# Kernel optimization log

Measured on AMD Instinct MI355X. Metric: run time of the kernel, lower is better.

Reference implementation:

```python
import jax, jax.numpy as jnp
import numpy as np

EPS = 1e-5


def _conv(x, w, padding, groups=1):
    return jax.lax.conv_general_dilated(
        x, w, window_strides=(1, 1),
        padding=[(padding, padding), (padding, padding)],
        dimension_numbers=("NCHW", "OIHW", "NCHW"),
        feature_group_count=groups)


def _bn(x, gamma, beta, mean, var):
    # inference-mode BatchNorm2d, params shape [C]
    inv = gamma * jax.lax.rsqrt(var + EPS)
    return x * inv[None, :, None, None] + (beta - mean * inv)[None, :, None, None]


def _adder_dw(x, w):
    # depthwise AdderNet 'conv': out[b, c*R+r, h, w] = -sum_{kh,kw} |x[b,c,h+kh-p,w+kw-p] - w[c,r,kh,kw]|
    # x: [B,C,H,W], w: [C,R,K,K] (groups=C, R outputs per group)
    B, C, H, W = x.shape
    R, K = w.shape[1], w.shape[-1]
    p = K // 2
    xp = jnp.pad(x, ((0, 0), (0, 0), (p, p), (p, p)))
    acc = jnp.zeros((B, C, R, H, W), x.dtype)
    for kh in range(K):          # fixed small 3x3 tap loop
        for kw in range(K):
            shift = xp[:, :, kh:kh + H, kw:kw + W]          # [B,C,H,W]
            tap = w[:, :, kh, kw]                           # [C,R]
            acc = acc + jnp.abs(shift[:, :, None] - tap[None, :, :, None, None])
    return -acc.reshape(B, C * R, H, W)


def setup_inputs() -> dict:
    key = jax.random.key(0)
    ks = jax.random.split(key, 12)
    B, Cin, H, W = 32, 240, 56, 56
    init_c, ratio = 24, 10
    r1 = ratio - 1            # 9 ghost channels per primary channel
    new_c = init_c * r1       # 216
    f32 = jnp.float32
    x = jax.random.normal(ks[0], (B, Cin, H, W), f32)
    w_primary = jax.random.normal(ks[1], (init_c, Cin, 1, 1), f32) * 0.05
    w_dw = jax.random.normal(ks[2], (init_c, 1, 3, 3), f32) * 0.1
    w_add = jax.random.normal(ks[3], (init_c, r1, 3, 3), f32) * 0.1
    def bn(kk, c):
        k1, k2 = jax.random.split(kk)
        return (jnp.ones((c,), f32), jnp.zeros((c,), f32),
                jax.random.normal(k1, (c,), f32) * 0.1,
                jax.random.uniform(k2, (c,), f32, 0.5, 1.5))
    g1, b1, m1, v1 = bn(ks[4], init_c)
    g2, b2, m2, v2 = bn(ks[5], init_c)
    g3, b3, m3, v3 = bn(ks[6], new_c)
    return dict(x=x, w_primary=w_primary, g1=g1, b1=b1, m1=m1, v1=v1,
                w_dw=w_dw, g2=g2, b2=b2, m2=m2, v2=v2,
                w_add=w_add, g3=g3, b3=b3, m3=m3, v3=v3)


def reference(x, w_primary, g1, b1, m1, v1, w_dw, g2, b2, m2, v2,
              w_add, g3, b3, m3, v3):
    oup = 240
    init_c = w_primary.shape[0]
    # primary_conv: 1x1 conv -> BN -> depthwise 3x3 conv -> BN -> Identity (relu slot is Identity)
    x1 = _conv(x, w_primary, padding=0)
    x1 = _bn(x1, g1, b1, m1, v1)
    x1 = _conv(x1, w_dw, padding=1, groups=init_c)
    x1 = _bn(x1, g2, b2, m2, v2)
    # cheap_operation: depthwise Adder2D -> BN -> ReLU
    x2 = _adder_dw(x1, w_add)
    x2 = jax.nn.relu(_bn(x2, g3, b3, m3, v3))
    out = jnp.concatenate([x1, x2], axis=1)
    return out[:, :oup]
```

## Files before the change

### kernel.cpp

```cpp
#include <hip/hip_runtime.h>

#define EPS_ 1e-5f
#define BATCH 32
#define CIN 240
#define H_ 56
#define W_ 56
#define HW 3136
#define C1 24
#define R_ 9
#define C2 216
#define COUT 240

#define WS_WT   0
#define WS_B1   5760
#define WS_WDW  5784
#define WS_B2   6000
#define WS_INV3 6024
#define WS_T3   6240

__global__ __launch_bounds__(256) void prep_kernel(
    const float* __restrict__ wp,
    const float* __restrict__ g1, const float* __restrict__ b1,
    const float* __restrict__ m1, const float* __restrict__ v1,
    const float* __restrict__ wdw,
    const float* __restrict__ g2, const float* __restrict__ b2,
    const float* __restrict__ m2, const float* __restrict__ v2,
    const float* __restrict__ g3, const float* __restrict__ b3,
    const float* __restrict__ m3, const float* __restrict__ v3,
    float* __restrict__ ws) {
  int i = blockIdx.x * 256 + threadIdx.x;
  if (i < 5760) {
    int ci = i / C1, co = i % C1;
    float s = g1[co] / sqrtf(v1[co] + EPS_);
    ws[WS_WT + ci * C1 + co] = wp[co * CIN + ci] * s;
    if (ci == 0) ws[WS_B1 + co] = b1[co] - m1[co] * s;
  } else if (i < 5760 + C2) {
    int j = i - 5760;
    int c = j / 9;
    float s = g2[c] / sqrtf(v2[c] + EPS_);
    ws[WS_WDW + j] = wdw[j] * s;
    if (j % 9 == 0) ws[WS_B2 + c] = b2[c] - m2[c] * s;
  } else if (i < 5976 + C2) {
    int j = i - 5976;
    float s = g3[j] / sqrtf(v3[j] + EPS_);
    ws[WS_INV3 + j] = s;
    ws[WS_T3 + j] = b3[j] - m3[j] * s;
  }
}

__global__ __launch_bounds__(256, 2) void conv1x1_kernel(
    const float* __restrict__ x, const float* __restrict__ wt,
    const float* __restrict__ bias1, float* __restrict__ out) {
  __shared__ float smem[12288];
  const int tid  = threadIdx.x;
  const int lane = tid & 63;
  const int wv   = tid >> 6;

  for (int i = tid; i < 5760; i += 256) smem[i] = wt[i];
  __syncthreads();

  const int P  = blockIdx.x * 256 + lane * 4;
  const int b  = P / HW;
  const int hw = P - b * HW;
  const int ci0 = wv * 60;
  const float* xp = x + ((size_t)b * CIN + ci0) * HW + hw;

  float acc[96];
#pragma unroll
  for (int i = 0; i < 96; ++i) acc[i] = 0.f;

  float4 A[6], B[6];
#pragma unroll
  for (int j = 0; j < 6; ++j) A[j] = *(const float4*)(xp + (size_t)j * HW);
#pragma unroll
  for (int j = 0; j < 6; ++j) B[j] = *(const float4*)(xp + (size_t)(6 + j) * HW);

  auto fmachunk = [&](const float4* buf, int cbase) {
#pragma unroll
    for (int j = 0; j < 6; ++j) {
      const float4 xv = buf[j];
      const float* wr = &smem[(ci0 + cbase + j) * C1];
#pragma unroll
      for (int k = 0; k < 6; ++k) {
        const float4 wq = *(const float4*)(wr + 4 * k);
        const int o = 16 * k;
        acc[o+ 0] = fmaf(wq.x, xv.x, acc[o+ 0]);
        acc[o+ 1] = fmaf(wq.x, xv.y, acc[o+ 1]);
        acc[o+ 2] = fmaf(wq.x, xv.z, acc[o+ 2]);
        acc[o+ 3] = fmaf(wq.x, xv.w, acc[o+ 3]);
        acc[o+ 4] = fmaf(wq.y, xv.x, acc[o+ 4]);
        acc[o+ 5] = fmaf(wq.y, xv.y, acc[o+ 5]);
        acc[o+ 6] = fmaf(wq.y, xv.z, acc[o+ 6]);
        acc[o+ 7] = fmaf(wq.y, xv.w, acc[o+ 7]);
        acc[o+ 8] = fmaf(wq.z, xv.x, acc[o+ 8]);
        acc[o+ 9] = fmaf(wq.z, xv.y, acc[o+ 9]);
        acc[o+10] = fmaf(wq.z, xv.z, acc[o+10]);
        acc[o+11] = fmaf(wq.z, xv.w, acc[o+11]);
        acc[o+12] = fmaf(wq.w, xv.x, acc[o+12]);
        acc[o+13] = fmaf(wq.w, xv.y, acc[o+13]);
        acc[o+14] = fmaf(wq.w, xv.z, acc[o+14]);
        acc[o+15] = fmaf(wq.w, xv.w, acc[o+15]);
      }
    }
  };

#pragma unroll 1
  for (int g = 0; g < 4; ++g) {
    const int c = 12 * g;
    fmachunk(A, c);
#pragma unroll
    for (int j = 0; j < 6; ++j)
      A[j] = *(const float4*)(xp + (size_t)(c + 12 + j) * HW);
    fmachunk(B, c + 6);
#pragma unroll
    for (int j = 0; j < 6; ++j)
      B[j] = *(const float4*)(xp + (size_t)(c + 18 + j) * HW);
  }
  fmachunk(A, 48);
  fmachunk(B, 54);
  __syncthreads();

  float* red0 = smem;
  float* red1 = smem + 6144;

  if (wv == 2) {
#pragma unroll
    for (int i = 0; i < 96; ++i) red0[i * 64 + lane] = acc[i];
  } else if (wv == 3) {
#pragma unroll
    for (int i = 0; i < 96; ++i) red1[i * 64 + lane] = acc[i];
  }
  __syncthreads();
  if (wv == 0) {
#pragma unroll
    for (int i = 0; i < 96; ++i) acc[i] += red0[i * 64 + lane];
  } else if (wv == 1) {
#pragma unroll
    for (int i = 0; i < 96; ++i) acc[i] += red1[i * 64 + lane];
  }
  __syncthreads();
  if (wv == 1) {
#pragma unroll
    for (int i = 0; i < 96; ++i) red0[i * 64 + lane] = acc[i];
  }
  __syncthreads();
  if (wv == 0) {
    float* o = out + ((size_t)b * COUT + C1) * HW + hw;
#pragma unroll
    for (int co = 0; co < C1; ++co) {
      const float bb = bias1[co];
      float4 v;
      v.x = acc[co*4+0] + red0[(co*4+0)*64 + lane] + bb;
      v.y = acc[co*4+1] + red0[(co*4+1)*64 + lane] + bb;
      v.z = acc[co*4+2] + red0[(co*4+2)*64 + lane] + bb;
      v.w = acc[co*4+3] + red0[(co*4+3)*64 + lane] + bb;
      *(float4*)(o + (size_t)co * HW) = v;
    }
  }
}

__global__ __launch_bounds__(256) void dw_kernel(
    const float* __restrict__ outr, const float* __restrict__ wdwf,
    const float* __restrict__ bias2, float* __restrict__ out) {
  const int c = blockIdx.y, b = blockIdx.z;
  const int q = blockIdx.x * 256 + threadIdx.x;
  if (q >= 784) return;
  const int h  = q / 14;
  const int w0 = (q - h * 14) * 4;
  const float* in = outr + ((size_t)b * COUT + C1 + c) * HW;

  float wk[9];
#pragma unroll
  for (int k = 0; k < 9; ++k) wk[k] = wdwf[c * 9 + k];
  const float bb = bias2[c];

  float xr[3][6];
#pragma unroll
  for (int kh = 0; kh < 3; ++kh) {
    const int hh = h + kh - 1;
    const bool rok = (hh >= 0) & (hh < H_);
    const float* rp = in + hh * W_;
    xr[kh][0] = (rok && w0 > 0) ? rp[w0 - 1] : 0.f;
    if (rok) {
      const float4 m = *(const float4*)(rp + w0);
      xr[kh][1] = m.x; xr[kh][2] = m.y; xr[kh][3] = m.z; xr[kh][4] = m.w;
    } else {
      xr[kh][1] = 0.f; xr[kh][2] = 0.f; xr[kh][3] = 0.f; xr[kh][4] = 0.f;
    }
    xr[kh][5] = (rok && w0 < W_ - 4) ? rp[w0 + 4] : 0.f;
  }

  float4 v = {bb, bb, bb, bb};
#pragma unroll
  for (int kh = 0; kh < 3; ++kh) {
#pragma unroll
    for (int kw = 0; kw < 3; ++kw) {
      const float t = wk[kh * 3 + kw];
      v.x = fmaf(xr[kh][kw + 0], t, v.x);
      v.y = fmaf(xr[kh][kw + 1], t, v.y);
      v.z = fmaf(xr[kh][kw + 2], t, v.z);
      v.w = fmaf(xr[kh][kw + 3], t, v.w);
    }
  }
  *(float4*)(out + ((size_t)b * COUT + c) * HW + h * W_ + w0) = v;
}

__global__ __launch_bounds__(256) void adder_kernel(
    const float* __restrict__ outr, const float* __restrict__ wadd,
    const float* __restrict__ inv3, const float* __restrict__ t3,
    float* __restrict__ out) {
  const int c = blockIdx.y, b = blockIdx.z;
  __shared__ float taps[R_][3][4];
  __shared__ float s3[R_], t3s[R_];
  const int tid = threadIdx.x;
  if (tid < 108) {
    int r = tid / 12, kh = (tid / 4) % 3, kw = tid & 3;
    taps[r][kh][kw] = (kw < 3) ? wadd[((c * R_ + r) * 3 + kh) * 3 + kw] : 0.f;
  } else if (tid >= 128 && tid < 128 + R_) {
    int r = tid - 128;
    s3[r]  = inv3[c * R_ + r];
    t3s[r] = t3[c * R_ + r];
  }
  __syncthreads();

  const int q = blockIdx.x * 256 + tid;
  if (q >= 784) return;
  const int h  = q / 14;
  const int w0 = (q - h * 14) * 4;
  const float* in = outr + ((size_t)b * COUT + c) * HW;

  float xr[3][6];
#pragma unroll
  for (int kh = 0; kh < 3; ++kh) {
    const int hh = h + kh - 1;
    const bool rok = (hh >= 0) & (hh < H_);
    const float* rp = in + hh * W_;
    xr[kh][0] = (rok && w0 > 0) ? rp[w0 - 1] : 0.f;
    if (rok) {
      const float4 m = *(const float4*)(rp + w0);
      xr[kh][1] = m.x; xr[kh][2] = m.y; xr[kh][3] = m.z; xr[kh][4] = m.w;
    } else {
      xr[kh][1] = 0.f; xr[kh][2] = 0.f; xr[kh][3] = 0.f; xr[kh][4] = 0.f;
    }
    xr[kh][5] = (rok && w0 < W_ - 4) ? rp[w0 + 4] : 0.f;
  }

#pragma unroll
  for (int r = 0; r < R_; ++r) {
    float a0 = 0.f, a1 = 0.f, a2 = 0.f, a3 = 0.f;
#pragma unroll
    for (int kh = 0; kh < 3; ++kh) {
#pragma unroll
      for (int kw = 0; kw < 3; ++kw) {
        const float t = taps[r][kh][kw];
        a0 += fabsf(xr[kh][kw + 0] - t);
        a1 += fabsf(xr[kh][kw + 1] - t);
        a2 += fabsf(xr[kh][kw + 2] - t);
        a3 += fabsf(xr[kh][kw + 3] - t);
      }
    }
    const float s = s3[r], bb = t3s[r];
    float4 v;
    v.x = fmaxf(fmaf(-s, a0, bb), 0.f);
    v.y = fmaxf(fmaf(-s, a1, bb), 0.f);
    v.z = fmaxf(fmaf(-s, a2, bb), 0.f);
    v.w = fmaxf(fmaf(-s, a3, bb), 0.f);
    *(float4*)(out + ((size_t)b * COUT + C1 + c * R_ + r) * HW + h * W_ + w0) = v;
  }
}

extern "C" void kernel_launch(void* const* d_in, const int* in_sizes, int n_in,
                              void* d_out, int out_size, void* d_ws, size_t ws_size,
                              hipStream_t stream) {
  const float* x    = (const float*)d_in[0];
  const float* wp   = (const float*)d_in[1];
  const float* g1   = (const float*)d_in[2];
  const float* b1   = (const float*)d_in[3];
  const float* m1   = (const float*)d_in[4];
  const float* v1   = (const float*)d_in[5];
  const float* wdw  = (const float*)d_in[6];
  const float* g2   = (const float*)d_in[7];
  const float* b2   = (const float*)d_in[8];
  const float* m2   = (const float*)d_in[9];
  const float* v2   = (const float*)d_in[10];
  const float* wadd = (const float*)d_in[11];
  const float* g3   = (const float*)d_in[12];
  const float* b3   = (const float*)d_in[13];
  const float* m3   = (const float*)d_in[14];
  const float* v3   = (const float*)d_in[15];

  float* ws  = (float*)d_ws;
  float* out = (float*)d_out;

  prep_kernel<<<25, 256, 0, stream>>>(wp, g1, b1, m1, v1, wdw, g2, b2, m2, v2,
                                      g3, b3, m3, v3, ws);

  conv1x1_kernel<<<392, 256, 0, stream>>>(x, ws + WS_WT, ws + WS_B1, out);

  dw_kernel<<<dim3(4, C1, BATCH), 256, 0, stream>>>(out, ws + WS_WDW,
                                                    ws + WS_B2, out);

  adder_kernel<<<dim3(4, C1, BATCH), 256, 0, stream>>>(out, wadd, ws + WS_INV3,
                                                       ws + WS_T3, out);
}
```

Measured before the change: 227.7 us.

## Split conv1x1 output channels across wave pairs to halve accumulators per thread

The 1x1 conv block grows from 256 to 512 threads. Each pair of waves shares one 60-channel K slice and splits the 24 output channels into two halves of 12, so each thread holds 48 accumulators instead of 96. Shared memory drops to 6144 floats and the launch bounds rise to (512,4), aiming for more resident waves to hide the global load latency on x. In exchange, every x value is loaded by two waves (doubling global/L2 reads of the input) and the cross-wave reduction takes more sync steps.

```diff
diff --git a/kernel.cpp b/kernel.cpp
--- a/kernel.cpp
+++ b/kernel.cpp
@@ -48,40 +48,43 @@
   }
 }
 
-__global__ __launch_bounds__(256, 2) void conv1x1_kernel(
+__global__ __launch_bounds__(512, 4) void conv1x1_kernel(
     const float* __restrict__ x, const float* __restrict__ wt,
     const float* __restrict__ bias1, float* __restrict__ out) {
-  __shared__ float smem[12288];
+  __shared__ float smem[6144];
   const int tid  = threadIdx.x;
   const int lane = tid & 63;
   const int wv   = tid >> 6;
-
-  for (int i = tid; i < 5760; i += 256) smem[i] = wt[i];
+  const int kq   = wv >> 1;
+  const int ch   = wv & 1;
+
+  for (int i = tid; i < 5760; i += 512) smem[i] = wt[i];
   __syncthreads();
 
   const int P  = blockIdx.x * 256 + lane * 4;
   const int b  = P / HW;
   const int hw = P - b * HW;
-  const int ci0 = wv * 60;
-  const float* xp = x + ((size_t)b * CIN + ci0) * HW + hw;
-
-  float acc[96];
-#pragma unroll
-  for (int i = 0; i < 96; ++i) acc[i] = 0.f;
-
-  float4 A[6], B[6];
-#pragma unroll
-  for (int j = 0; j < 6; ++j) A[j] = *(const float4*)(xp + (size_t)j * HW);
-#pragma unroll
-  for (int j = 0; j < 6; ++j) B[j] = *(const float4*)(xp + (size_t)(6 + j) * HW);
-
-  auto fmachunk = [&](const float4* buf, int cbase) {
-#pragma unroll
-    for (int j = 0; j < 6; ++j) {
+  const int ci0 = kq * 60;
+  const float* xp    = x + ((size_t)b * CIN + ci0) * HW + hw;
+  const float* wbase = smem + ci0 * C1 + ch * 12;
+
+  float acc[48];
+#pragma unroll
+  for (int i = 0; i < 48; ++i) acc[i] = 0.f;
+
+  float4 A[5], B[5];
+#pragma unroll
+  for (int j = 0; j < 5; ++j) A[j] = *(const float4*)(xp + (size_t)j * HW);
+#pragma unroll
+  for (int j = 0; j < 5; ++j) B[j] = *(const float4*)(xp + (size_t)(5 + j) * HW);
+
+  auto consume = [&](const float4* buf, int cb) {
+#pragma unroll
+    for (int j = 0; j < 5; ++j) {
       const float4 xv = buf[j];
-      const float* wr = &smem[(ci0 + cbase + j) * C1];
-#pragma unroll
-      for (int k = 0; k < 6; ++k) {
+      const float* wr = wbase + (cb + j) * C1;
+#pragma unroll
+      for (int k = 0; k < 3; ++k) {
         const float4 wq = *(const float4*)(wr + 4 * k);
         const int o = 16 * k;
         acc[o+ 0] = fmaf(wq.x, xv.x, acc[o+ 0]);
@@ -105,55 +108,58 @@
   };
 
 #pragma unroll 1
-  for (int g = 0; g < 4; ++g) {
-    const int c = 12 * g;
-    fmachunk(A, c);
-#pragma unroll
-    for (int j = 0; j < 6; ++j)
-      A[j] = *(const float4*)(xp + (size_t)(c + 12 + j) * HW);
-    fmachunk(B, c + 6);
-#pragma unroll
-    for (int j = 0; j < 6; ++j)
-      B[j] = *(const float4*)(xp + (size_t)(c + 18 + j) * HW);
-  }
-  fmachunk(A, 48);
-  fmachunk(B, 54);
-  __syncthreads();
-
-  float* red0 = smem;
-  float* red1 = smem + 6144;
-
-  if (wv == 2) {
-#pragma unroll
-    for (int i = 0; i < 96; ++i) red0[i * 64 + lane] = acc[i];
-  } else if (wv == 3) {
-#pragma unroll
-    for (int i = 0; i < 96; ++i) red1[i * 64 + lane] = acc[i];
-  }
-  __syncthreads();
-  if (wv == 0) {
-#pragma unroll
-    for (int i = 0; i < 96; ++i) acc[i] += red0[i * 64 + lane];
-  } else if (wv == 1) {
-#pragma unroll
-    for (int i = 0; i < 96; ++i) acc[i] += red1[i * 64 + lane];
-  }
-  __syncthreads();
-  if (wv == 1) {
-#pragma unroll
-    for (int i = 0; i < 96; ++i) red0[i * 64 + lane] = acc[i];
-  }
-  __syncthreads();
-  if (wv == 0) {
-    float* o = out + ((size_t)b * COUT + C1) * HW + hw;
-#pragma unroll
-    for (int co = 0; co < C1; ++co) {
-      const float bb = bias1[co];
+  for (int g = 0; g < 5; ++g) {
+    const int c = 10 * g;
+    consume(A, c);
+#pragma unroll
+    for (int j = 0; j < 5; ++j)
+      A[j] = *(const float4*)(xp + (size_t)(c + 10 + j) * HW);
+    consume(B, c + 5);
+#pragma unroll
+    for (int j = 0; j < 5; ++j)
+      B[j] = *(const float4*)(xp + (size_t)(c + 15 + j) * HW);
+  }
+  consume(A, 50);
+  consume(B, 55);
+  __syncthreads();
+
+  float* red = smem + ch * 3072;
+
+  if (kq == 3) {
+#pragma unroll
+    for (int i = 0; i < 48; ++i) red[i * 64 + lane] = acc[i];
+  }
+  __syncthreads();
+  if (kq == 1) {
+#pragma unroll
+    for (int i = 0; i < 48; ++i) acc[i] += red[i * 64 + lane];
+  }
+  __syncthreads();
+  if (kq == 2) {
+#pragma unroll
+    for (int i = 0; i < 48; ++i) red[i * 64 + lane] = acc[i];
+  }
+  __syncthreads();
+  if (kq == 0) {
+#pragma unroll
+    for (int i = 0; i < 48; ++i) acc[i] += red[i * 64 + lane];
+  }
+  __syncthreads();
+  if (kq == 1) {
+#pragma unroll
+    for (int i = 0; i < 48; ++i) red[i * 64 + lane] = acc[i];
+  }
+  __syncthreads();
+  if (kq == 0) {
+    float* o = out + ((size_t)b * COUT + C1 + ch * 12) * HW + hw;
+#pragma unroll
+    for (int co = 0; co < 12; ++co) {
+      const float bb = bias1[ch * 12 + co];
       float4 v;
-      v.x = acc[co*4+0] + red0[(co*4+0)*64 + lane] + bb;
-      v.y = acc[co*4+1] + red0[(co*4+1)*64 + lane] + bb;
-      v.z = acc[co*4+2] + red0[(co*4+2)*64 + lane] + bb;
-      v.w = acc[co*4+3] + red0[(co*4+3)*64 + lane] + bb;
+      v.x = acc[co*4+0] + red[(co*4+0)*64 + lane] + bb;
+      v.y = acc[co*4+1] + red[(co*4+1)*64 + lane] + bb;
+      v.z = acc[co*4+2] + red[(co*4+2)*64 + lane] + bb;
+      v.w = acc[co*4+3] + red[(co*4+3)*64 + lane] + bb;
       *(float4*)(o + (size_t)co * HW) = v;
     }
   }
@@ -295,7 +301,7 @@
   prep_kernel<<<25, 256, 0, stream>>>(wp, g1, b1, m1, v1, wdw, g2, b2, m2, v2,
                                       g3, b3, m3, v3, ws);
 
-  conv1x1_kernel<<<392, 256, 0, stream>>>(x, ws + WS_WT, ws + WS_B1, out);
+  conv1x1_kernel<<<392, 512, 0, stream>>>(x, ws + WS_WT, ws + WS_B1, out);
 
   dw_kernel<<<dim3(4, C1, BATCH), 256, 0, stream>>>(out, ws + WS_WDW,
                                                     ws + WS_B2, out);
```

After: 241.8 us. 1.06x slower.

## Shrink conv1x1 per-thread tile to one pixel and parallelize split-K reduction

Applied to the files above, without the earlier changes.

The 1x1 conv kernel now computes one pixel per thread (24 accumulators instead of 96) with float loads instead of float4. The grid grows fourfold to 1568 blocks. The cross-wave K reduction is now spread over all four waves, each summing 6 output channels from shared memory. The goal is less register pressure, higher occupancy and more blocks to hide memory latency. The cost is scalar global loads and less weight reuse per LDS read.

```diff
diff --git a/kernel.cpp b/kernel.cpp
--- a/kernel.cpp
+++ b/kernel.cpp
@@ -48,58 +48,46 @@
   }
 }
 
-__global__ __launch_bounds__(256, 2) void conv1x1_kernel(
+__global__ __launch_bounds__(256) void conv1x1_kernel(
     const float* __restrict__ x, const float* __restrict__ wt,
     const float* __restrict__ bias1, float* __restrict__ out) {
-  __shared__ float smem[12288];
+  __shared__ float smem[6144];
   const int tid  = threadIdx.x;
   const int lane = tid & 63;
-  const int wv   = tid >> 6;
+  const int kq   = tid >> 6;
 
   for (int i = tid; i < 5760; i += 256) smem[i] = wt[i];
   __syncthreads();
 
-  const int P  = blockIdx.x * 256 + lane * 4;
-  const int b  = P / HW;
-  const int hw = P - b * HW;
-  const int ci0 = wv * 60;
-  const float* xp = x + ((size_t)b * CIN + ci0) * HW + hw;
-
-  float acc[96];
-#pragma unroll
-  for (int i = 0; i < 96; ++i) acc[i] = 0.f;
-
-  float4 A[6], B[6];
-#pragma unroll
-  for (int j = 0; j < 6; ++j) A[j] = *(const float4*)(xp + (size_t)j * HW);
-#pragma unroll
-  for (int j = 0; j < 6; ++j) B[j] = *(const float4*)(xp + (size_t)(6 + j) * HW);
-
-  auto fmachunk = [&](const float4* buf, int cbase) {
+  const int P   = blockIdx.x * 64 + lane;
+  const int b   = P / HW;
+  const int hw  = P - b * HW;
+  const int ci0 = kq * 60;
+  const float* xp    = x + ((size_t)b * CIN + ci0) * HW + hw;
+  const float* wbase = smem + ci0 * C1;
+
+  float acc[C1];
+#pragma unroll
+  for (int i = 0; i < C1; ++i) acc[i] = 0.f;
+
+  float A[6], B[6];
+#pragma unroll
+  for (int j = 0; j < 6; ++j) A[j] = xp[(size_t)j * HW];
+#pragma unroll
+  for (int j = 0; j < 6; ++j) B[j] = xp[(size_t)(6 + j) * HW];
+
+  auto consume = [&](const float* buf, int cb) {
 #pragma unroll
     for (int j = 0; j < 6; ++j) {
-      const float4 xv = buf[j];
-      const float* wr = &smem[(ci0 + cbase + j) * C1];
+      const float xv = buf[j];
+      const float* wr = wbase + (cb + j) * C1;
 #pragma unroll
       for (int k = 0; k < 6; ++k) {
         const float4 wq = *(const float4*)(wr + 4 * k);
-        const int o = 16 * k;
-        acc[o+ 0] = fmaf(wq.x, xv.x, acc[o+ 0]);
-        acc[o+ 1] = fmaf(wq.x, xv.y, acc[o+ 1]);
-        acc[o+ 2] = fmaf(wq.x, xv.z, acc[o+ 2]);
-        acc[o+ 3] = fmaf(wq.x, xv.w, acc[o+ 3]);
-        acc[o+ 4] = fmaf(wq.y, xv.x, acc[o+ 4]);
-        acc[o+ 5] = fmaf(wq.y, xv.y, acc[o+ 5]);
-        acc[o+ 6] = fmaf(wq.y, xv.z, acc[o+ 6]);
-        acc[o+ 7] = fmaf(wq.y, xv.w, acc[o+ 7]);
-        acc[o+ 8] = fmaf(wq.z, xv.x, acc[o+ 8]);
-        acc[o+ 9] = fmaf(wq.z, xv.y, acc[o+ 9]);
-        acc[o+10] = fmaf(wq.z, xv.z, acc[o+10]);
-        acc[o+11] = fmaf(wq.z, xv.w, acc[o+11]);
-        acc[o+12] = fmaf(wq.w, xv.x, acc[o+12]);
-        acc[o+13] = fmaf(wq.w, xv.y, acc[o+13]);
-        acc[o+14] = fmaf(wq.w, xv.z, acc[o+14]);
-        acc[o+15] = fmaf(wq.w, xv.w, acc[o+15]);
+        acc[4*k+0] = fmaf(wq.x, xv, acc[4*k+0]);
+        acc[4*k+1] = fmaf(wq.y, xv, acc[4*k+1]);
+        acc[4*k+2] = fmaf(wq.z, xv, acc[4*k+2]);
+        acc[4*k+3] = fmaf(wq.w, xv, acc[4*k+3]);
       }
     }
   };
@@ -107,55 +95,31 @@
 #pragma unroll 1
   for (int g = 0; g < 4; ++g) {
     const int c = 12 * g;
-    fmachunk(A, c);
-#pragma unroll
-    for (int j = 0; j < 6; ++j)
-      A[j] = *(const float4*)(xp + (size_t)(c + 12 + j) * HW);
-    fmachunk(B, c + 6);
-#pragma unroll
-    for (int j = 0; j < 6; ++j)
-      B[j] = *(const float4*)(xp + (size_t)(c + 18 + j) * HW);
-  }
-  fmachunk(A, 48);
-  fmachunk(B, 54);
-  __syncthreads();
-
-  float* red0 = smem;
-  float* red1 = smem + 6144;
-
-  if (wv == 2) {
-#pragma unroll
-    for (int i = 0; i < 96; ++i) red0[i * 64 + lane] = acc[i];
-  } else if (wv == 3) {
-#pragma unroll
-    for (int i = 0; i < 96; ++i) red1[i * 64 + lane] = acc[i];
-  }
-  __syncthreads();
-  if (wv == 0) {
-#pragma unroll
-    for (int i = 0; i < 96; ++i) acc[i] += red0[i * 64 + lane];
-  } else if (wv == 1) {
-#pragma unroll
-    for (int i = 0; i < 96; ++i) acc[i] += red1[i * 64 + lane];
-  }
-  __syncthreads();
-  if (wv == 1) {
-#pragma unroll
-    for (int i = 0; i < 96; ++i) red0[i * 64 + lane] = acc[i];
-  }
-  __syncthreads();
-  if (wv == 0) {
-    float* o = out + ((size_t)b * COUT + C1) * HW + hw;
-#pragma unroll
-    for (int co = 0; co < C1; ++co) {
-      const float bb = bias1[co];
-      float4 v;
-      v.x = acc[co*4+0] + red0[(co*4+0)*64 + lane] + bb;
-      v.y = acc[co*4+1] + red0[(co*4+1)*64 + lane] + bb;
-      v.z = acc[co*4+2] + red0[(co*4+2)*64 + lane] + bb;
-      v.w = acc[co*4+3] + red0[(co*4+3)*64 + lane] + bb;
-      *(float4*)(o + (size_t)co * HW) = v;
-    }
+    consume(A, c);
+#pragma unroll
+    for (int j = 0; j < 6; ++j) A[j] = xp[(size_t)(c + 12 + j) * HW];
+    consume(B, c + 6);
+#pragma unroll
+    for (int j = 0; j < 6; ++j) B[j] = xp[(size_t)(c + 18 + j) * HW];
+  }
+  consume(A, 48);
+  consume(B, 54);
+  __syncthreads();
+
+#pragma unroll
+  for (int i = 0; i < C1; ++i) smem[(kq * C1 + i) * 64 + lane] = acc[i];
+  __syncthreads();
+
+  float* o = out + ((size_t)b * COUT + C1) * HW + hw;
+#pragma unroll
+  for (int i = 0; i < 6; ++i) {
+    const int co = kq * 6 + i;
+    float v = smem[(0 * C1 + co) * 64 + lane]
+            + smem[(1 * C1 + co) * 64 + lane]
+            + smem[(2 * C1 + co) * 64 + lane]
+            + smem[(3 * C1 + co) * 64 + lane]
+            + bias1[co];
+    o[(size_t)co * HW] = v;
   }
 }
 
@@ -295,7 +259,7 @@
   prep_kernel<<<25, 256, 0, stream>>>(wp, g1, b1, m1, v1, wdw, g2, b2, m2, v2,
                                       g3, b3, m3, v3, ws);
 
-  conv1x1_kernel<<<392, 256, 0, stream>>>(x, ws + WS_WT, ws + WS_B1, out);
+  conv1x1_kernel<<<1568, 256, 0, stream>>>(x, ws + WS_WT, ws + WS_B1, out);
 
   dw_kernel<<<dim3(4, C1, BATCH), 256, 0, stream>>>(out, ws + WS_WDW,
                                                     ws + WS_B2, out);
```

Result: faster. 217.6 us (-4.4%).
